# Kernel optimization log

Measured on AMD Instinct MI355X. Metric: run time of the kernel, lower is better.

Reference implementation:

```python
import jax, jax.numpy as jnp
import numpy as np


def _rotate_half(x):
    half = x.shape[-1] // 2
    x1, x2 = x[..., :half], x[..., half:]
    return jnp.concatenate([-x2, x1], axis=-1)


def setup_inputs() -> dict:
    key = jax.random.key(0)
    ks = jax.random.split(key, 7)
    B, T, D, H, Hd = 4, 2048, 1024, 16, 64
    x = jax.random.normal(ks[0], (B, T, D), dtype=jnp.float32)
    # RoPE tables (realistic: built from inv freqs)
    inv_freq = 1.0 / (10000.0 ** (jnp.arange(0, Hd, 2, dtype=jnp.float32) / Hd))
    pos = jnp.arange(T, dtype=jnp.float32)
    freqs = pos[:, None] * inv_freq[None, :]            # (T, Hd/2)
    emb = jnp.concatenate([freqs, freqs], axis=-1)       # (T, Hd)
    cos, sin = jnp.cos(emb), jnp.sin(emb)
    s = 1.0 / np.sqrt(D)
    w_q = jax.random.normal(ks[1], (D, D), dtype=jnp.float32) * s
    w_k = jax.random.normal(ks[2], (D, D), dtype=jnp.float32) * s
    w_v = jax.random.normal(ks[3], (D, D), dtype=jnp.float32) * s
    w_o = jax.random.normal(ks[4], (D, D), dtype=jnp.float32) * s
    return {"x": x, "cos": cos, "sin": sin, "w_q": w_q, "w_k": w_k, "w_v": w_v, "w_o": w_o}


def reference(x, cos, sin, w_q, w_k, w_v, w_o):
    B, T, D = x.shape
    H = 16
    Hd = D // H
    scale = Hd ** -0.5
    # nn.Linear(bias=False): y = x @ W.T
    q = (x @ w_q.T).reshape(B, T, H, Hd).transpose(0, 2, 1, 3)  # (B,H,T,Hd)
    k = (x @ w_k.T).reshape(B, T, H, Hd).transpose(0, 2, 1, 3)
    v = (x @ w_v.T).reshape(B, T, H, Hd).transpose(0, 2, 1, 3)
    c = cos[None, None, :, :]
    s = sin[None, None, :, :]
    q = q * c + _rotate_half(q) * s
    k = k * c + _rotate_half(k) * s
    scores = jnp.einsum('bhqd,bhkd->bhqk', q, k) * scale  # (B,H,T,T)
    causal = jnp.tril(jnp.ones((T, T), dtype=bool))
    scores = jnp.where(causal[None, None], scores, -jnp.inf)
    weights = jax.nn.softmax(scores, axis=-1)
    out = jnp.einsum('bhqk,bhkd->bhqd', weights, v)
    out = out.transpose(0, 2, 1, 3).reshape(B, T, D)
    return out @ w_o.T
```

## Files before the change

### kernel.cpp

```cpp
#include <hip/hip_runtime.h>
#include <stdint.h>

typedef __attribute__((ext_vector_type(8))) __bf16 bf16x8;
typedef __attribute__((ext_vector_type(4))) float floatx4;


__device__ __forceinline__ unsigned short f2bf(float f) {
    unsigned int u = __float_as_uint(f);
    u += 0x7FFFu + ((u >> 16) & 1u);
    return (unsigned short)(u >> 16);
}
__device__ __forceinline__ unsigned int pack2bf(float lo, float hi) {
    return (unsigned int)f2bf(lo) | ((unsigned int)f2bf(hi) << 16);
}
__device__ __forceinline__ unsigned int packtrunc(float lo, float hi) {
    return __builtin_amdgcn_perm(__float_as_uint(hi), __float_as_uint(lo), 0x07060302u);
}

__device__ __forceinline__ void gl_lds16(const void* g, void* l) {
    __builtin_amdgcn_global_load_lds(
        (const __attribute__((address_space(1))) void*)g,
        (__attribute__((address_space(3))) void*)l, 16, 0, 0);
}


__global__ void cvt_all(const float* __restrict__ x,  const float* __restrict__ wq,
                        const float* __restrict__ wk, const float* __restrict__ wv,
                        const float* __restrict__ wo,
                        unsigned short* __restrict__ xb,  unsigned short* __restrict__ wqb,
                        unsigned short* __restrict__ wkb, unsigned short* __restrict__ wvb,
                        unsigned short* __restrict__ wob) {
    int i = blockIdx.x * blockDim.x + threadIdx.x;
    const float* in; unsigned short* out; int idx;
    if (i < 2097152) { in = x; out = xb; idx = i; }
    else {
        int j = i - 2097152; int wsel = j >> 18; idx = j & 262143;
        in  = (wsel == 0) ? wq  : (wsel == 1) ? wk  : (wsel == 2) ? wv  : wo;
        out = (wsel == 0) ? wqb : (wsel == 1) ? wkb : (wsel == 2) ? wvb : wob;
    }
    float4 v = ((const float4*)in)[idx];
    ushort4 o;
    o.x = f2bf(v.x); o.y = f2bf(v.y); o.z = f2bf(v.z); o.w = f2bf(v.w);
    ((ushort4*)out)[idx] = o;
}


template<int MODE>
__global__ __launch_bounds__(256, 2)
void gemm_bt(const unsigned short* __restrict__ A,
             const unsigned short* __restrict__ Wq,
             const unsigned short* __restrict__ Wk,
             const unsigned short* __restrict__ Wv,
             const float* __restrict__ cosp,
             const float* __restrict__ sinp,
             unsigned short* __restrict__ outq,
             unsigned short* __restrict__ outk,
             unsigned short* __restrict__ outvt,
             float* __restrict__ outf)
{
    constexpr int K = 1024;
    __shared__ __align__(16) unsigned short As[128 * 64];
    __shared__ __align__(16) unsigned short Bs[128 * 64];

    const int t    = threadIdx.x;
    const int w    = t >> 6;
    const int lane = t & 63;
    const int c    = lane & 15;
    const int quad = lane >> 4;
    const int wr   = w >> 1, wc = w & 1;

    const int m0 = blockIdx.x * 128;
    int which3, n0;
    const unsigned short* W;
    if constexpr (MODE == 0) {
        which3 = blockIdx.y >> 3;
        n0     = (blockIdx.y & 7) * 128;
        W      = (which3 == 0) ? Wq : (which3 == 1) ? Wk : Wv;
    } else {
        which3 = 0;
        n0     = blockIdx.y * 128;
        W      = Wq;
    }
    const bool vmode = (MODE == 0) && (which3 == 2);

    const int srow = t >> 3;
    const int sj   = ((t & 7) ^ (srow & 7)) * 8;
    const unsigned short* ga[4];
    const unsigned short* gb[4];
    #pragma unroll
    for (int j = 0; j < 4; j++) {
        ga[j] = A + (size_t)(m0 + srow + 32 * j) * K + sj;
        gb[j] = W + (size_t)(n0 + srow + 32 * j) * K + sj;
    }

    floatx4 acc[4][4] = {};

    const int arow = wr * 64;
    const int brow = wc * 64;

    for (int k0 = 0; k0 < K; k0 += 64) {
        __syncthreads();
        #pragma unroll
        for (int j = 0; j < 4; j++) {
            gl_lds16(ga[j] + k0, (char*)As + j * 4096 + t * 16);
            gl_lds16(gb[j] + k0, (char*)Bs + j * 4096 + t * 16);
        }
        __syncthreads();
        #pragma unroll
        for (int kk = 0; kk < 2; kk++) {
            const int phys = (((kk << 2) | quad) ^ (c & 7)) * 8;
            bf16x8 af[4], bfr[4];
            #pragma unroll
            for (int mi = 0; mi < 4; mi++)
                af[mi] = *(const bf16x8*)&As[(arow + mi * 16 + c) * 64 + phys];
            #pragma unroll
            for (int ni = 0; ni < 4; ni++)
                bfr[ni] = *(const bf16x8*)&Bs[(brow + ni * 16 + c) * 64 + phys];
            if (vmode) {
                #pragma unroll
                for (int mi = 0; mi < 4; mi++)
                    #pragma unroll
                    for (int ni = 0; ni < 4; ni++)
                        acc[mi][ni] = __builtin_amdgcn_mfma_f32_16x16x32_bf16(
                            af[mi], bfr[ni], acc[mi][ni], 0, 0, 0);
            } else {
                #pragma unroll
                for (int mi = 0; mi < 4; mi++)
                    #pragma unroll
                    for (int ni = 0; ni < 4; ni++)
                        acc[mi][ni] = __builtin_amdgcn_mfma_f32_16x16x32_bf16(
                            bfr[ni], af[mi], acc[mi][ni], 0, 0, 0);
            }
        }
    }

    if constexpr (MODE == 1) {
        #pragma unroll
        for (int mi = 0; mi < 4; mi++) {
            int m = m0 + wr * 64 + mi * 16 + c;
            #pragma unroll
            for (int ni = 0; ni < 4; ni++) {
                int n = n0 + wc * 64 + ni * 16 + quad * 4;
                *(floatx4*)&outf[(size_t)m * 1024 + n] = acc[mi][ni];
            }
        }
    } else if (vmode) {
        const int hh = (n0 + wc * 64) >> 6;
        #pragma unroll
        for (int mi = 0; mi < 4; mi++) {
            int t0 = m0 + wr * 64 + mi * 16 + quad * 4;
            int b = t0 >> 11, tt0 = t0 & 2047;
            #pragma unroll
            for (int ni = 0; ni < 4; ni++) {
                int d = ni * 16 + c;
                uint2 pk;
                pk.x = pack2bf(acc[mi][ni][0], acc[mi][ni][1]);
                pk.y = pack2bf(acc[mi][ni][2], acc[mi][ni][3]);
                *(uint2*)&outvt[((size_t)((b * 16 + hh) * 64 + d)) * 2048 + tt0] = pk;
            }
        }
    } else {
        const int hh = (n0 + wc * 64) >> 6;
        unsigned short* dst = which3 ? outk : outq;
        const float scale = which3 ? 1.0f : (0.125f * 1.44269504088896f);
        #pragma unroll
        for (int mi = 0; mi < 4; mi++) {
            int m = m0 + wr * 64 + mi * 16 + c;
            int b = m >> 11, tt = m & 2047;
            size_t obase = ((size_t)(b * 16 + hh) * 2048 + tt) * 64;
            #pragma unroll
            for (int ni = 0; ni < 4; ni++) {
                int d0 = ni * 16 + quad * 4;
                float4 cv = *(const float4*)&cosp[tt * 64 + d0];
                float4 sv = *(const float4*)&sinp[tt * 64 + d0];
                float ca[4] = {cv.x, cv.y, cv.z, cv.w};
                float sa[4] = {sv.x, sv.y, sv.z, sv.w};
                float vq[4];
                #pragma unroll
                for (int r = 0; r < 4; r++) {
                    float pr  = acc[mi][ni ^ 2][r];
                    float rot = (ni & 2) ? pr : -pr;
                    vq[r] = (acc[mi][ni][r] * ca[r] + rot * sa[r]) * scale;
                }
                uint2 pk;
                pk.x = pack2bf(vq[0], vq[1]);
                pk.y = pack2bf(vq[2], vq[3]);
                *(uint2*)&dst[obase + d0] = pk;
            }
        }
    }
}

__global__ __launch_bounds__(256)
void flash_attn(const unsigned short* __restrict__ Q,
                const unsigned short* __restrict__ Kg,
                const unsigned short* __restrict__ Vt,
                unsigned short* __restrict__ O)
{
    __shared__ __align__(16) unsigned short Ks[2][64 * 64];
    __shared__ __align__(16) unsigned short Vs[2][64 * 64];

    const int t    = threadIdx.x;
    const int w    = t >> 6;
    const int lane = t & 63;
    const int c    = lane & 15;
    const int quad = lane >> 4;

    const int bh = blockIdx.x;
    const int b  = bh >> 4, h = bh & 15;

    const unsigned short* qp = Q  + (size_t)bh * 2048 * 64;
    const unsigned short* kp = Kg + (size_t)bh * 2048 * 64;
    const unsigned short* vp = Vt + (size_t)bh * 64 * 2048;

    const int srow = t >> 3;
    const int sj   = (t & 7) ^ (srow & 7);

    const int qi = 31 - (int)blockIdx.y;
    const int q0 = qi * 64;
    const int qb = q0 + w * 16;

    bf16x8 qf[2];
    #pragma unroll
    for (int dc = 0; dc < 2; dc++)
        qf[dc] = *(const bf16x8*)&qp[(size_t)(qb + c) * 64 + dc * 32 + quad * 8];

    union { unsigned short us[8]; bf16x8 v; } one8;
    #pragma unroll
    for (int j = 0; j < 8; j++) one8.us[j] = 0x3F80;

    floatx4 o[4] = {};
    floatx4 lacc = {};

    #pragma unroll
    for (int ch = 0; ch < 2; ch++) {
        int kr = ch * 32 + srow;
        gl_lds16(kp + (size_t)kr * 64 + sj * 8, (char*)&Ks[0][0] + ch * 4096 + t * 16);
        gl_lds16(vp + (size_t)kr * 2048 + sj * 8, (char*)&Vs[0][0] + ch * 4096 + t * 16);
    }

    const int iters = qi + 1;
    for (int it = 0; it < iters; it++) {
        const int cur = it & 1;
        const int kt0 = it * 64;
        __syncthreads();
        if (it + 1 < iters) {
            const int kt1 = kt0 + 64;
            #pragma unroll
            for (int ch = 0; ch < 2; ch++) {
                int kr = ch * 32 + srow;
                gl_lds16(kp + (size_t)(kt1 + kr) * 64 + sj * 8,
                         (char*)&Ks[cur ^ 1][0] + ch * 4096 + t * 16);
                gl_lds16(vp + (size_t)kr * 2048 + kt1 + sj * 8,
                         (char*)&Vs[cur ^ 1][0] + ch * 4096 + t * 16);
            }
        }
        const unsigned short* KsC = &Ks[cur][0];
        const unsigned short* VsC = &Vs[cur][0];

        floatx4 s[4] = {};
        #pragma unroll
        for (int dc = 0; dc < 2; dc++) {
            const int phys = (dc * 4 + quad) ^ (c & 7);
            #pragma unroll
            for (int mt = 0; mt < 4; mt++) {
                bf16x8 kb = *(const bf16x8*)&KsC[(mt * 16 + c) * 64 + phys * 8];
                s[mt] = __builtin_amdgcn_mfma_f32_16x16x32_bf16(kb, qf[dc], s[mt], 0, 0, 0);
            }
        }

        if (it == iters - 1) {
            #pragma unroll
            for (int mt = 0; mt < 4; mt++) {
                int keyb = kt0 + mt * 16 + quad * 4;
                #pragma unroll
                for (int r = 0; r < 4; r++)
                    if (keyb + r > qb + c) s[mt][r] = -1e30f;
            }
        }

        uint2 pk[4];
        #pragma unroll
        for (int mt = 0; mt < 4; mt++) {
            float p0 = __builtin_amdgcn_exp2f(s[mt][0]);
            float p1 = __builtin_amdgcn_exp2f(s[mt][1]);
            float p2 = __builtin_amdgcn_exp2f(s[mt][2]);
            float p3 = __builtin_amdgcn_exp2f(s[mt][3]);
            pk[mt].x = packtrunc(p0, p1);
            pk[mt].y = packtrunc(p2, p3);
        }

        #pragma unroll
        for (int kc = 0; kc < 2; kc++) {
            unsigned int x0 = pk[2 * kc].x;
            unsigned int x1 = pk[2 * kc].y;
            unsigned int x2 = pk[2 * kc + 1].x;
            unsigned int x3 = pk[2 * kc + 1].y;
            asm("v_permlane32_swap_b32 %0, %1" : "+v"(x0), "+v"(x2));
            asm("v_permlane32_swap_b32 %0, %1" : "+v"(x1), "+v"(x3));
            asm("v_permlane16_swap_b32 %0, %1" : "+v"(x0), "+v"(x2));
            asm("v_permlane16_swap_b32 %0, %1" : "+v"(x1), "+v"(x3));
            union { unsigned int u[4]; bf16x8 v; } ap;
            ap.u[0] = x0; ap.u[1] = x1; ap.u[2] = x2; ap.u[3] = x3;

            lacc = __builtin_amdgcn_mfma_f32_16x16x32_bf16(ap.v, one8.v, lacc, 0, 0, 0);

            const int phys = (kc * 4 + quad) ^ (c & 7);
            #pragma unroll
            for (int ni = 0; ni < 4; ni++) {
                bf16x8 vb = *(const bf16x8*)&VsC[(ni * 16 + c) * 64 + phys * 8];
                o[ni] = __builtin_amdgcn_mfma_f32_16x16x32_bf16(ap.v, vb, o[ni], 0, 0, 0);
            }
        }
    }

    #pragma unroll
    for (int r = 0; r < 4; r++) {
        float linv = __builtin_amdgcn_rcpf(lacc[r]);
        int qrow = qb + quad * 4 + r;
        size_t base = ((size_t)(b * 2048 + qrow)) * 1024 + h * 64;
        #pragma unroll
        for (int ni = 0; ni < 4; ni++)
            O[base + ni * 16 + c] = f2bf(o[ni][r] * linv);
    }
}


extern "C" void kernel_launch(void* const* d_in, const int* in_sizes, int n_in,
                              void* d_out, int out_size, void* d_ws, size_t ws_size,
                              hipStream_t stream) {
    const float* x    = (const float*)d_in[0];
    const float* cosp = (const float*)d_in[1];
    const float* sinp = (const float*)d_in[2];
    const float* wq   = (const float*)d_in[3];
    const float* wk   = (const float*)d_in[4];
    const float* wv   = (const float*)d_in[5];
    const float* wo   = (const float*)d_in[6];

    char* ws = (char*)d_ws;
    const size_t MB = 1024 * 1024;
    unsigned short* xb   = (unsigned short*)(ws + 0);
    unsigned short* attn = (unsigned short*)(ws + 0);
    unsigned short* wqb  = (unsigned short*)(ws + 16 * MB);
    unsigned short* wkb  = (unsigned short*)(ws + 18 * MB);
    unsigned short* wvb  = (unsigned short*)(ws + 20 * MB);
    unsigned short* wob  = (unsigned short*)(ws + 22 * MB);
    unsigned short* qbuf = (unsigned short*)(ws + 24 * MB);
    unsigned short* kbuf = (unsigned short*)(ws + 40 * MB);
    unsigned short* vtb  = (unsigned short*)(ws + 56 * MB);

    cvt_all<<<dim3(12288), 256, 0, stream>>>(x, wq, wk, wv, wo,
                                             xb, wqb, wkb, wvb, wob);

    gemm_bt<0><<<dim3(64, 24), 256, 0, stream>>>(xb, wqb, wkb, wvb, cosp, sinp,
                                                 qbuf, kbuf, vtb, nullptr);

    flash_attn<<<dim3(64, 32), 256, 0, stream>>>(qbuf, kbuf, vtb, attn);

    gemm_bt<1><<<dim3(64, 8), 256, 0, stream>>>(attn, wob, nullptr, nullptr, nullptr, nullptr,
                                                nullptr, nullptr, nullptr, (float*)d_out);
}
```

Baseline: 243.8 us.

## Rework QKV GEMM with 256-row tiles and triple-buffered async LDS pipeline

The fused QKV projection kernel becomes a separate kernel with 256x128 block tiles, K-step 32, and a three-stage LDS ring. Loads for step it+2 are issued while step it computes, using explicit vmcnt waits and a single barrier per step instead of two syncthreads. MFMA sections are wrapped in setprio. The output GEMM is split into its own non-templated copy of the old kernel. The risks are higher register pressure from 32 accumulators per thread, and the unswizzled 32-wide LDS rows may cause bank conflicts.

```diff
diff --git a/kernel.cpp b/kernel.cpp
--- a/kernel.cpp
+++ b/kernel.cpp
@@ -45,22 +45,21 @@
 }
 
 
-template<int MODE>
 __global__ __launch_bounds__(256, 2)
-void gemm_bt(const unsigned short* __restrict__ A,
-             const unsigned short* __restrict__ Wq,
-             const unsigned short* __restrict__ Wk,
-             const unsigned short* __restrict__ Wv,
-             const float* __restrict__ cosp,
-             const float* __restrict__ sinp,
-             unsigned short* __restrict__ outq,
-             unsigned short* __restrict__ outk,
-             unsigned short* __restrict__ outvt,
-             float* __restrict__ outf)
+void gemm_qkv8(const unsigned short* __restrict__ A,
+               const unsigned short* __restrict__ Wq,
+               const unsigned short* __restrict__ Wk,
+               const unsigned short* __restrict__ Wv,
+               const float* __restrict__ cosp,
+               const float* __restrict__ sinp,
+               unsigned short* __restrict__ outq,
+               unsigned short* __restrict__ outk,
+               unsigned short* __restrict__ outvt)
 {
-    constexpr int K = 1024;
-    __shared__ __align__(16) unsigned short As[128 * 64];
-    __shared__ __align__(16) unsigned short Bs[128 * 64];
+    constexpr int K  = 1024;
+    constexpr int NT = 32;
+    __shared__ __align__(16) unsigned short As[3][256 * 32];
+    __shared__ __align__(16) unsigned short Bs[3][128 * 32];
 
     const int t    = threadIdx.x;
     const int w    = t >> 6;
@@ -69,86 +68,74 @@
     const int quad = lane >> 4;
     const int wr   = w >> 1, wc = w & 1;
 
-    const int m0 = blockIdx.x * 128;
-    int which3, n0;
-    const unsigned short* W;
-    if constexpr (MODE == 0) {
-        which3 = blockIdx.y >> 3;
-        n0     = (blockIdx.y & 7) * 128;
-        W      = (which3 == 0) ? Wq : (which3 == 1) ? Wk : Wv;
-    } else {
-        which3 = 0;
-        n0     = blockIdx.y * 128;
-        W      = Wq;
-    }
-    const bool vmode = (MODE == 0) && (which3 == 2);
-
-    const int srow = t >> 3;
-    const int sj   = ((t & 7) ^ (srow & 7)) * 8;
-    const unsigned short* ga[4];
-    const unsigned short* gb[4];
-    #pragma unroll
-    for (int j = 0; j < 4; j++) {
-        ga[j] = A + (size_t)(m0 + srow + 32 * j) * K + sj;
-        gb[j] = W + (size_t)(n0 + srow + 32 * j) * K + sj;
-    }
-
-    floatx4 acc[4][4] = {};
-
-    const int arow = wr * 64;
-    const int brow = wc * 64;
-
-    for (int k0 = 0; k0 < K; k0 += 64) {
-        __syncthreads();
-        #pragma unroll
-        for (int j = 0; j < 4; j++) {
-            gl_lds16(ga[j] + k0, (char*)As + j * 4096 + t * 16);
-            gl_lds16(gb[j] + k0, (char*)Bs + j * 4096 + t * 16);
-        }
-        __syncthreads();
-        #pragma unroll
-        for (int kk = 0; kk < 2; kk++) {
-            const int phys = (((kk << 2) | quad) ^ (c & 7)) * 8;
-            bf16x8 af[4], bfr[4];
-            #pragma unroll
-            for (int mi = 0; mi < 4; mi++)
-                af[mi] = *(const bf16x8*)&As[(arow + mi * 16 + c) * 64 + phys];
-            #pragma unroll
-            for (int ni = 0; ni < 4; ni++)
-                bfr[ni] = *(const bf16x8*)&Bs[(brow + ni * 16 + c) * 64 + phys];
-            if (vmode) {
+    const int m0     = blockIdx.x * 256;
+    const int which3 = blockIdx.y >> 3;
+    const int n0     = (blockIdx.y & 7) * 128;
+    const unsigned short* W = (which3 == 0) ? Wq : (which3 == 1) ? Wk : Wv;
+
+    const int srow = t >> 2;
+    const int scol = (t & 3) * 8;
+    const unsigned short* gA = A + (size_t)(m0 + srow) * K + scol;
+    const unsigned short* gB = W + (size_t)(n0 + srow) * K + scol;
+
+    auto stage = [&](int buf, int k0) {
+        char* la = (char*)&As[buf][0] + t * 16;
+        #pragma unroll
+        for (int j = 0; j < 4; j++)
+            gl_lds16(gA + (size_t)(64 * j) * K + k0, la + j * 4096);
+        char* lb = (char*)&Bs[buf][0] + t * 16;
+        #pragma unroll
+        for (int j = 0; j < 2; j++)
+            gl_lds16(gB + (size_t)(64 * j) * K + k0, lb + j * 4096);
+    };
+
+    floatx4 acc[8][4] = {};
+
+    stage(0, 0);
+    stage(1, 32);
+
+    for (int it = 0; it < NT; ++it) {
+        if (it < NT - 1) asm volatile("s_waitcnt vmcnt(6) lgkmcnt(0)" ::: "memory");
+        else             asm volatile("s_waitcnt vmcnt(0) lgkmcnt(0)" ::: "memory");
+        __builtin_amdgcn_s_barrier();
+        __builtin_amdgcn_sched_barrier(0);
+
+        if (it + 2 < NT) stage((it + 2) % 3, (it + 2) * 32);
+
+        const unsigned short* AsC = &As[it % 3][0];
+        const unsigned short* BsC = &Bs[it % 3][0];
+        bf16x8 af[8], bfr[4];
+        #pragma unroll
+        for (int mi = 0; mi < 8; mi++)
+            af[mi] = *(const bf16x8*)&AsC[(wr * 128 + mi * 16 + c) * 32 + quad * 8];
+        #pragma unroll
+        for (int ni = 0; ni < 4; ni++)
+            bfr[ni] = *(const bf16x8*)&BsC[(wc * 64 + ni * 16 + c) * 32 + quad * 8];
+
+        __builtin_amdgcn_s_setprio(1);
+        if (which3 == 2) {
+            #pragma unroll
+            for (int mi = 0; mi < 8; mi++)
                 #pragma unroll
-                for (int mi = 0; mi < 4; mi++)
-                    #pragma unroll
-                    for (int ni = 0; ni < 4; ni++)
-                        acc[mi][ni] = __builtin_amdgcn_mfma_f32_16x16x32_bf16(
-                            af[mi], bfr[ni], acc[mi][ni], 0, 0, 0);
-            } else {
+                for (int ni = 0; ni < 4; ni++)
+                    acc[mi][ni] = __builtin_amdgcn_mfma_f32_16x16x32_bf16(
+                        af[mi], bfr[ni], acc[mi][ni], 0, 0, 0);
+        } else {
+            #pragma unroll
+            for (int mi = 0; mi < 8; mi++)
                 #pragma unroll
-                for (int mi = 0; mi < 4; mi++)
-                    #pragma unroll
-                    for (int ni = 0; ni < 4; ni++)
-                        acc[mi][ni] = __builtin_amdgcn_mfma_f32_16x16x32_bf16(
-                            bfr[ni], af[mi], acc[mi][ni], 0, 0, 0);
-            }
-        }
-    }
-
-    if constexpr (MODE == 1) {
-        #pragma unroll
-        for (int mi = 0; mi < 4; mi++) {
-            int m = m0 + wr * 64 + mi * 16 + c;
-            #pragma unroll
-            for (int ni = 0; ni < 4; ni++) {
-                int n = n0 + wc * 64 + ni * 16 + quad * 4;
-                *(floatx4*)&outf[(size_t)m * 1024 + n] = acc[mi][ni];
-            }
-        }
-    } else if (vmode) {
+                for (int ni = 0; ni < 4; ni++)
+                    acc[mi][ni] = __builtin_amdgcn_mfma_f32_16x16x32_bf16(
+                        bfr[ni], af[mi], acc[mi][ni], 0, 0, 0);
+        }
+        __builtin_amdgcn_s_setprio(0);
+    }
+
+    if (which3 == 2) {
         const int hh = (n0 + wc * 64) >> 6;
         #pragma unroll
-        for (int mi = 0; mi < 4; mi++) {
-            int t0 = m0 + wr * 64 + mi * 16 + quad * 4;
+        for (int mi = 0; mi < 8; mi++) {
+            int t0 = m0 + wr * 128 + mi * 16 + quad * 4;
             int b = t0 >> 11, tt0 = t0 & 2047;
             #pragma unroll
             for (int ni = 0; ni < 4; ni++) {
@@ -164,8 +151,8 @@
         unsigned short* dst = which3 ? outk : outq;
         const float scale = which3 ? 1.0f : (0.125f * 1.44269504088896f);
         #pragma unroll
-        for (int mi = 0; mi < 4; mi++) {
-            int m = m0 + wr * 64 + mi * 16 + c;
+        for (int mi = 0; mi < 8; mi++) {
+            int m = m0 + wr * 128 + mi * 16 + c;
             int b = m >> 11, tt = m & 2047;
             size_t obase = ((size_t)(b * 16 + hh) * 2048 + tt) * 64;
             #pragma unroll
@@ -191,6 +178,79 @@
     }
 }
 
+
+__global__ __launch_bounds__(256, 2)
+void gemm_out(const unsigned short* __restrict__ A,
+              const unsigned short* __restrict__ Wo,
+              float* __restrict__ outf)
+{
+    constexpr int K = 1024;
+    __shared__ __align__(16) unsigned short As[128 * 64];
+    __shared__ __align__(16) unsigned short Bs[128 * 64];
+
+    const int t    = threadIdx.x;
+    const int w    = t >> 6;
+    const int lane = t & 63;
+    const int c    = lane & 15;
+    const int quad = lane >> 4;
+    const int wr   = w >> 1, wc = w & 1;
+
+    const int m0 = blockIdx.x * 128;
+    const int n0 = blockIdx.y * 128;
+
+    const int srow = t >> 3;
+    const int sj   = ((t & 7) ^ (srow & 7)) * 8;
+    const unsigned short* ga[4];
+    const unsigned short* gb[4];
+    #pragma unroll
+    for (int j = 0; j < 4; j++) {
+        ga[j] = A  + (size_t)(m0 + srow + 32 * j) * K + sj;
+        gb[j] = Wo + (size_t)(n0 + srow + 32 * j) * K + sj;
+    }
+
+    floatx4 acc[4][4] = {};
+
+    const int arow = wr * 64;
+    const int brow = wc * 64;
+
+    for (int k0 = 0; k0 < K; k0 += 64) {
+        __syncthreads();
+        #pragma unroll
+        for (int j = 0; j < 4; j++) {
+            gl_lds16(ga[j] + k0, (char*)As + j * 4096 + t * 16);
+            gl_lds16(gb[j] + k0, (char*)Bs + j * 4096 + t * 16);
+        }
+        __syncthreads();
+        #pragma unroll
+        for (int kk = 0; kk < 2; kk++) {
+            const int phys = (((kk << 2) | quad) ^ (c & 7)) * 8;
+            bf16x8 af[4], bfr[4];
+            #pragma unroll
+            for (int mi = 0; mi < 4; mi++)
+                af[mi] = *(const bf16x8*)&As[(arow + mi * 16 + c) * 64 + phys];
+            #pragma unroll
+            for (int ni = 0; ni < 4; ni++)
+                bfr[ni] = *(const bf16x8*)&Bs[(brow + ni * 16 + c) * 64 + phys];
+            #pragma unroll
+            for (int mi = 0; mi < 4; mi++)
+                #pragma unroll
+                for (int ni = 0; ni < 4; ni++)
+                    acc[mi][ni] = __builtin_amdgcn_mfma_f32_16x16x32_bf16(
+                        bfr[ni], af[mi], acc[mi][ni], 0, 0, 0);
+        }
+    }
+
+    #pragma unroll
+    for (int mi = 0; mi < 4; mi++) {
+        int m = m0 + wr * 64 + mi * 16 + c;
+        #pragma unroll
+        for (int ni = 0; ni < 4; ni++) {
+            int n = n0 + wc * 64 + ni * 16 + quad * 4;
+            *(floatx4*)&outf[(size_t)m * 1024 + n] = acc[mi][ni];
+        }
+    }
+}
+
 __global__ __launch_bounds__(256)
 void flash_attn(const unsigned short* __restrict__ Q,
                 const unsigned short* __restrict__ Kg,
@@ -352,11 +412,10 @@
     cvt_all<<<dim3(12288), 256, 0, stream>>>(x, wq, wk, wv, wo,
                                              xb, wqb, wkb, wvb, wob);
 
-    gemm_bt<0><<<dim3(64, 24), 256, 0, stream>>>(xb, wqb, wkb, wvb, cosp, sinp,
-                                                 qbuf, kbuf, vtb, nullptr);
+    gemm_qkv8<<<dim3(32, 24), 256, 0, stream>>>(xb, wqb, wkb, wvb, cosp, sinp,
+                                                qbuf, kbuf, vtb);
 
     flash_attn<<<dim3(64, 32), 256, 0, stream>>>(qbuf, kbuf, vtb, attn);
 
-    gemm_bt<1><<<dim3(64, 8), 256, 0, stream>>>(attn, wob, nullptr, nullptr, nullptr, nullptr,
-                                                nullptr, nullptr, nullptr, (float*)d_out);
-}
+    gemm_out<<<dim3(64, 8), 256, 0, stream>>>(attn, wob, (float*)d_out);
+}
```

Result: slower. 549.5 us (+125.4%).
